# Kernel optimization log

Hardware: AMD Instinct MI355X
Metric: run time of the kernel (lower is better)

Reference implementation:

```python
import jax, jax.numpy as jnp
import numpy as np

_EPS = 1e-5

def _ln(x, g, b):
    m = jnp.mean(x, axis=-1, keepdims=True)
    v = jnp.var(x, axis=-1, keepdims=True)
    return (x - m) * jax.lax.rsqrt(v + _EPS) * g + b

def setup_inputs() -> dict:
    key = jax.random.key(0)
    ks = jax.random.split(key, 12)
    B, S, D = 8, 2048, 1024
    H = 2 * D          # hidden_dim = 2*n_embd
    A = H // 16        # adapt_dim = 128
    E = 8              # num_experts
    std = 1.0 / D ** 0.5
    astd = std * 0.01
    f = lambda k, shape, s: jax.random.normal(k, shape, dtype=jnp.float32) * s
    return {
        'x': f(ks[0], (B, S, D), 1.0),
        'expert_weights': f(ks[1], (B, S, E), 1.0),
        'w_up': f(ks[2], (H, D), std),
        'w_gate': f(ks[3], (H, D), std),
        'w_down': f(ks[4], (D, H), std),
        'w_pre': f(ks[5], (A, D), astd),
        'w_post': f(ks[6], (A, H), astd),
        'an_g': jnp.ones((A,), jnp.float32),
        'an_b': jnp.zeros((A,), jnp.float32),
        'w_aproj': f(ks[7], (H, A), astd),
        'w_exp': f(ks[8], (E, A, A), 0.01 / A ** 0.5),
        'eln_g': jnp.ones((E, A), jnp.float32),
        'eln_b': jnp.zeros((E, A), jnp.float32),
        'w_eproj': f(ks[9], (H, A), 0.01 / A ** 0.5),
        'w_out': f(ks[10], (D, H), 0.01 / A ** 0.5),
    }

def reference(x, expert_weights, w_up, w_gate, w_down, w_pre, w_post,
              an_g, an_b, w_aproj, w_exp, eln_g, eln_b, w_eproj, w_out):
    # ---- shared LLaDAExpert ----
    up = jnp.einsum('bsd,hd->bsh', x, w_up)
    gate = jnp.einsum('bsd,hd->bsh', x, w_gate)
    hidden = jax.nn.silu(gate) * up                      # [B,S,H]
    pre = jnp.einsum('bsd,ad->bsa', x, w_pre)            # pre_adapt(x), reused by experts
    adapt_in = _ln(pre, an_g, an_b)                      # [B,S,A]
    adapt_out = _ln(jnp.einsum('bsh,ah->bsa', hidden, w_post), an_g, an_b)
    aw = jax.nn.silu(jnp.clip(jnp.einsum('bsa,bta->bst', adapt_in, adapt_out), -5.0, 5.0))  # [B,S,S]
    adapt = jnp.einsum('bst,bta->bsa', aw, adapt_in)     # [B,S,A]
    hidden = hidden + 0.1 * jnp.einsum('bsa,ha->bsh', adapt, w_aproj)
    shared = jnp.einsum('bsh,dh->bsd', hidden, w_down)   # [B,S,D]
    combined = jnp.zeros_like(shared)
    E = w_exp.shape[0]
    for i in range(E):
        a = _ln(jnp.einsum('bsa,ca->bsc', pre, w_exp[i]), eln_g[i], eln_b[i])
        o = jnp.einsum('bsh,dh->bsd', jnp.einsum('bsc,hc->bsh', a, w_eproj), w_out)
        mask = expert_weights[:, :, i] > 0
        combined = jnp.where(mask[..., None], o, combined)
    return shared + 0.1 * combined
```

## Files before the change

kernel.cpp:

```cpp
#include <hip/hip_runtime.h>

#define TOK 16384
#define DD 1024
#define HH 2048
#define AA 128
#define EE 8
#define SS 2048
#define BB 8

typedef __attribute__((ext_vector_type(8))) short short8;
typedef __attribute__((ext_vector_type(4))) float floatx4;
typedef __attribute__((address_space(1))) const void glob_cvoid;
typedef __attribute__((address_space(3))) void lds_void;

__device__ __forceinline__ unsigned short f2b(float f) {
  unsigned u = __float_as_uint(f);
  u += 0x7fff + ((u >> 16) & 1);
  return (unsigned short)(u >> 16);
}
__device__ __forceinline__ float b2f(unsigned short h) {
  return __uint_as_float(((unsigned)h) << 16);
}

__device__ __forceinline__ void xcd_swizzle(int& bx, int& by) {
  const int nbx = gridDim.x, nby = gridDim.y;
  if ((nby & 7) == 0) {
    const int L = blockIdx.y * nbx + blockIdx.x;
    const int xcd = L & 7, idx = L >> 3;
    bx = idx % nbx;
    by = (xcd * (nby >> 3)) + idx / nbx;
  } else {
    bx = blockIdx.x; by = blockIdx.y;
  }
}

__global__ void cast_f32_bf16(const float* __restrict__ in, unsigned short* __restrict__ out, long n4) {
  long i = (long)blockIdx.x * blockDim.x + threadIdx.x;
  const long stride = (long)gridDim.x * blockDim.x;
  for (; i < n4; i += stride) {
    float4 v = ((const float4*)in)[i];
    ushort4 o;
    o.x = f2b(v.x); o.y = f2b(v.y); o.z = f2b(v.z); o.w = f2b(v.w);
    ((ushort4*)out)[i] = o;
  }
}

__global__ void transpose_cast(const float* __restrict__ in, unsigned short* __restrict__ out,
                               int R, int C) {
  __shared__ float t[32][33];
  const int lx = threadIdx.x & 31, ly = threadIdx.x >> 5;
  const int r0 = blockIdx.y * 32, c0 = blockIdx.x * 32;
#pragma unroll
  for (int i = 0; i < 32; i += 8)
    t[ly + i][lx] = in[(long)(r0 + ly + i) * C + (c0 + lx)];
  __syncthreads();
#pragma unroll
  for (int i = 0; i < 32; i += 8)
    out[(long)(c0 + ly + i) * R + (r0 + lx)] = f2b(t[lx][ly + i]);
}

template<int EPI>
__global__ __launch_bounds__(256)
void gemm_bt(const unsigned short* __restrict__ Ag, long sAz, int lda,
             const unsigned short* __restrict__ Bg, long sBz, int ldb,
             void* __restrict__ Cg, long sCz, int ldc,
             const unsigned short* __restrict__ Xg, long sXz, int ldx,
             int K)
{
  __shared__ __align__(16) short As[128*64];
  __shared__ __align__(16) short Bs[128*64];
  int bx, by; xcd_swizzle(bx, by);
  const int tid  = threadIdx.x;
  const int lane = tid & 63, wave = tid >> 6;
  const int q = lane >> 4, l15 = lane & 15, l7 = lane & 7;
  const int wm = wave & 1, wn = wave >> 1;

  const int arow = tid >> 3;
  const int kc8  = ((tid & 7) ^ (arow & 7)) * 8;

  const short* Ap = (const short*)Ag + (long)blockIdx.z*sAz + (long)(by*128 + arow)*lda + kc8;
  const short* Bp = (const short*)Bg + (long)blockIdx.z*sBz + (long)(bx*128 + arow)*ldb + kc8;
  char* AsW = (char*)As + wave*1024;
  char* BsW = (char*)Bs + wave*1024;

  floatx4 acc[4][4] = {};

  for (int kt = 0; kt < K; kt += 64) {
    __syncthreads();
#pragma unroll
    for (int i = 0; i < 4; ++i) {
      __builtin_amdgcn_global_load_lds((glob_cvoid*)(Ap + (long)i*32*lda + kt),
                                       (lds_void*)(AsW + i*4096), 16, 0, 0);
      __builtin_amdgcn_global_load_lds((glob_cvoid*)(Bp + (long)i*32*ldb + kt),
                                       (lds_void*)(BsW + i*4096), 16, 0, 0);
    }
    __syncthreads();
#pragma unroll
    for (int s = 0; s < 2; ++s) {
      short8 af[4], bf[4];
      const int slotoff = ((s*4 + q) ^ l7) * 16;
#pragma unroll
      for (int i = 0; i < 4; ++i) {
        af[i] = *(const short8*)((const char*)As + (wm*64 + i*16 + l15)*128 + slotoff);
        bf[i] = *(const short8*)((const char*)Bs + (wn*64 + i*16 + l15)*128 + slotoff);
      }
#pragma unroll
      for (int i = 0; i < 4; ++i)
#pragma unroll
        for (int j = 0; j < 4; ++j)
          acc[i][j] = __builtin_amdgcn_mfma_f32_16x16x32_bf16(af[i], bf[j], acc[i][j], 0, 0, 0);
    }
  }

  const long cz = (long)blockIdx.z * sCz;
  const long xz = (long)blockIdx.z * sXz;
#pragma unroll
  for (int i = 0; i < 4; ++i)
#pragma unroll
    for (int j = 0; j < 4; ++j)
#pragma unroll
      for (int r = 0; r < 4; ++r) {
        const int row = by*128 + wm*64 + i*16 + q*4 + r;
        const int col = bx*128 + wn*64 + j*16 + l15;
        const long ci = cz + (long)row*ldc + col;
        float v = acc[i][j][r];
        if (EPI == 0) {
          ((float*)Cg)[ci] = v;
        } else if (EPI == 1) {
          v = v / (1.f + __expf(-v));
          ((unsigned short*)Cg)[ci] = f2b(v);
        } else if (EPI == 2) {
          float g = b2f(Xg[xz + (long)row*ldx + col]);
          ((unsigned short*)Cg)[ci] = f2b(v * g);
        } else if (EPI == 3) {
          ((unsigned short*)Cg)[ci] = f2b(v);
        } else if (EPI == 4) {
          v = fminf(fmaxf(v, -5.f), 5.f);
          v = v / (1.f + __expf(-v));
          ((unsigned short*)Cg)[ci] = f2b(v);
        } else if (EPI == 6) {
          ((unsigned short*)Cg)[ci] = f2b(0.1f * v);
        }
      }
}

__global__ __launch_bounds__(256)
void gemm_final(const unsigned short* __restrict__ hidp,
                const unsigned short* __restrict__ wdbp,
                const unsigned short* __restrict__ Fcp,
                const unsigned short* __restrict__ Wcp,
                float* __restrict__ outp)
{
  __shared__ __align__(16) short As[128*64];
  __shared__ __align__(16) short Bs[128*64];
  int bx, by; xcd_swizzle(bx, by);
  const int tid  = threadIdx.x;
  const int lane = tid & 63, wave = tid >> 6;
  const int q = lane >> 4, l15 = lane & 15, l7 = lane & 7;
  const int wm = wave & 1, wn = wave >> 1;
  const int arow = tid >> 3;
  const int kc8  = ((tid & 7) ^ (arow & 7)) * 8;
  char* AsW = (char*)As + wave*1024;
  char* BsW = (char*)Bs + wave*1024;

  floatx4 acc[4][4] = {};

  {
    const short* Ap = (const short*)hidp + (long)(by*128 + arow)*HH + kc8;
    const short* Bp = (const short*)wdbp + (long)(bx*128 + arow)*HH + kc8;
    for (int kt = 0; kt < HH; kt += 64) {
      __syncthreads();
#pragma unroll
      for (int i = 0; i < 4; ++i) {
        __builtin_amdgcn_global_load_lds((glob_cvoid*)(Ap + (long)i*32*HH + kt),
                                         (lds_void*)(AsW + i*4096), 16, 0, 0);
        __builtin_amdgcn_global_load_lds((glob_cvoid*)(Bp + (long)i*32*HH + kt),
                                         (lds_void*)(BsW + i*4096), 16, 0, 0);
      }
      __syncthreads();
#pragma unroll
      for (int s = 0; s < 2; ++s) {
        short8 af[4], bf[4];
        const int slotoff = ((s*4 + q) ^ l7) * 16;
#pragma unroll
        for (int i = 0; i < 4; ++i) {
          af[i] = *(const short8*)((const char*)As + (wm*64 + i*16 + l15)*128 + slotoff);
          bf[i] = *(const short8*)((const char*)Bs + (wn*64 + i*16 + l15)*128 + slotoff);
        }
#pragma unroll
        for (int i = 0; i < 4; ++i)
#pragma unroll
          for (int j = 0; j < 4; ++j)
            acc[i][j] = __builtin_amdgcn_mfma_f32_16x16x32_bf16(af[i], bf[j], acc[i][j], 0, 0, 0);
      }
    }
  }
  {
    const short* Ap = (const short*)Fcp + (long)(by*128 + arow)*256 + kc8;
    const short* Bp = (const short*)Wcp + (long)(bx*128 + arow)*256 + kc8;
    for (int kt = 0; kt < 256; kt += 64) {
      __syncthreads();
#pragma unroll
      for (int i = 0; i < 4; ++i) {
        __builtin_amdgcn_global_load_lds((glob_cvoid*)(Ap + (long)i*32*256 + kt),
                                         (lds_void*)(AsW + i*4096), 16, 0, 0);
        __builtin_amdgcn_global_load_lds((glob_cvoid*)(Bp + (long)i*32*256 + kt),
                                         (lds_void*)(BsW + i*4096), 16, 0, 0);
      }
      __syncthreads();
#pragma unroll
      for (int s = 0; s < 2; ++s) {
        short8 af[4], bf[4];
        const int slotoff = ((s*4 + q) ^ l7) * 16;
#pragma unroll
        for (int i = 0; i < 4; ++i) {
          af[i] = *(const short8*)((const char*)As + (wm*64 + i*16 + l15)*128 + slotoff);
          bf[i] = *(const short8*)((const char*)Bs + (wn*64 + i*16 + l15)*128 + slotoff);
        }
#pragma unroll
        for (int i = 0; i < 4; ++i)
#pragma unroll
          for (int j = 0; j < 4; ++j)
            acc[i][j] = __builtin_amdgcn_mfma_f32_16x16x32_bf16(af[i], bf[j], acc[i][j], 0, 0, 0);
      }
    }
  }

#pragma unroll
  for (int i = 0; i < 4; ++i)
#pragma unroll
    for (int j = 0; j < 4; ++j)
#pragma unroll
      for (int r = 0; r < 4; ++r) {
        const int row = by*128 + wm*64 + i*16 + q*4 + r;
        const int col = bx*128 + wn*64 + j*16 + l15;
        outp[(long)row*DD + col] = acc[i][j][r];
      }
}

__global__ void ln_rows(const float* __restrict__ X, const float* __restrict__ g,
                        const float* __restrict__ b, unsigned short* __restrict__ lnout,
                        unsigned short* __restrict__ rawout, unsigned short* __restrict__ tout)
{
  const int lane = threadIdx.x & 63, wave = threadIdx.x >> 6;
  const long t = (long)blockIdx.x*4 + wave;
  const float* x = X + t*AA;
  float x0 = x[lane], x1 = x[lane + 64];
  float s = x0 + x1, s2 = x0*x0 + x1*x1;
#pragma unroll
  for (int m = 1; m < 64; m <<= 1) {
    s  += __shfl_xor(s, m, 64);
    s2 += __shfl_xor(s2, m, 64);
  }
  float mean = s * (1.f/AA);
  float inv  = rsqrtf(s2*(1.f/AA) - mean*mean + 1e-5f);
  float y0 = (x0 - mean)*inv*g[lane] + b[lane];
  float y1 = (x1 - mean)*inv*g[lane+64] + b[lane+64];
  lnout[t*AA + lane]      = f2b(y0);
  lnout[t*AA + lane + 64] = f2b(y1);
  if (rawout) { rawout[t*AA+lane] = f2b(x0); rawout[t*AA+lane+64] = f2b(x1); }
  if (tout) {
    const long bb = t >> 11, si = t & (SS-1);
    tout[bb*(long)AA*SS + (long)lane*SS + si]      = f2b(y0);
    tout[bb*(long)AA*SS + (long)(lane+64)*SS + si] = f2b(y1);
  }
}

__global__ void expert_select_ln(const float* __restrict__ ew, const unsigned short* __restrict__ eall,
                                 const float* __restrict__ eg, const float* __restrict__ ebias,
                                 unsigned short* __restrict__ Fc)
{
  const int lane = threadIdx.x & 63, wave = threadIdx.x >> 6;
  const long t = (long)blockIdx.x*4 + wave;
  const float* w = ew + t*EE;
  int ie = -1;
#pragma unroll
  for (int i = 0; i < EE; ++i) if (w[i] > 0.f) ie = i;
  unsigned short o0 = 0, o1 = 0;
  if (ie >= 0) {
    float x0 = b2f(eall[t*(EE*AA) + ie*AA + lane]);
    float x1 = b2f(eall[t*(EE*AA) + ie*AA + lane + 64]);
    float s = x0 + x1, s2 = x0*x0 + x1*x1;
#pragma unroll
    for (int m = 1; m < 64; m <<= 1) { s += __shfl_xor(s, m, 64); s2 += __shfl_xor(s2, m, 64); }
    float mean = s * (1.f/AA);
    float inv  = rsqrtf(s2*(1.f/AA) - mean*mean + 1e-5f);
    o0 = f2b((x0-mean)*inv*eg[ie*AA+lane]    + ebias[ie*AA+lane]);
    o1 = f2b((x1-mean)*inv*eg[ie*AA+lane+64] + ebias[ie*AA+lane+64]);
  }
  Fc[t*256 + lane]      = o0;
  Fc[t*256 + lane + 64] = o1;
}

extern "C" void kernel_launch(void* const* d_in, const int* in_sizes, int n_in,
                              void* d_out, int out_size, void* d_ws, size_t ws_size,
                              hipStream_t stream)
{
  const float* x       = (const float*)d_in[0];
  const float* ew      = (const float*)d_in[1];
  const float* w_up    = (const float*)d_in[2];
  const float* w_gate  = (const float*)d_in[3];
  const float* w_down  = (const float*)d_in[4];
  const float* w_pre   = (const float*)d_in[5];
  const float* w_post  = (const float*)d_in[6];
  const float* an_g    = (const float*)d_in[7];
  const float* an_b    = (const float*)d_in[8];
  const float* w_aproj = (const float*)d_in[9];
  const float* w_exp   = (const float*)d_in[10];
  const float* eln_g   = (const float*)d_in[11];
  const float* eln_b   = (const float*)d_in[12];
  const float* w_eproj = (const float*)d_in[13];
  const float* w_out   = (const float*)d_in[14];

  char* ws = (char*)d_ws;
  size_t off = 0;
  auto take = [&](size_t bytes) { char* p = ws + off; off += (bytes + 255) & ~(size_t)255; return p; };

  unsigned short* Sc    = (unsigned short*)take((size_t)BB*SS*SS*2);
  unsigned short* xb    = Sc;
  unsigned short* eall  = (unsigned short*)((char*)Sc + (size_t)TOK*DD*2);
  unsigned short* hid   = (unsigned short*)take((size_t)TOK*HH*2);
  float*          pre   = (float*)take((size_t)TOK*AA*4);
  float*          postA = (float*)take((size_t)TOK*AA*4);
  unsigned short* Fc    = (unsigned short*)take((size_t)TOK*256*2);
  unsigned short* ain   = (unsigned short*)take((size_t)TOK*AA*2);
  unsigned short* ainT  = (unsigned short*)take((size_t)TOK*AA*2);
  unsigned short* aout  = (unsigned short*)take((size_t)TOK*AA*2);
  unsigned short* preb  = (unsigned short*)take((size_t)TOK*AA*2);
  unsigned short* wgb   = (unsigned short*)take((size_t)HH*DD*2);
  unsigned short* wub   = (unsigned short*)take((size_t)HH*DD*2);
  unsigned short* wdb   = (unsigned short*)take((size_t)DD*HH*2);
  unsigned short* wpostb= (unsigned short*)take((size_t)AA*HH*2);
  unsigned short* wpreb = (unsigned short*)take((size_t)AA*DD*2);
  unsigned short* wexpb = (unsigned short*)take((size_t)EE*AA*AA*2);
  unsigned short* Wc    = (unsigned short*)take((size_t)DD*256*2);
  (void)ws_size; (void)in_sizes; (void)n_in; (void)out_size;

  unsigned short* woutb  = hid;
  unsigned short* btT    = hid + (size_t)DD*HH;
  unsigned short* eprojT = btT;
  unsigned short* aprojT = btT + (size_t)AA*HH;

  cast_f32_bf16<<<1024, 256, 0, stream>>>(x,      xb,     (long)TOK*DD/4);
  cast_f32_bf16<<<256,  256, 0, stream>>>(w_gate, wgb,    (long)HH*DD/4);
  cast_f32_bf16<<<256,  256, 0, stream>>>(w_up,   wub,    (long)HH*DD/4);
  cast_f32_bf16<<<256,  256, 0, stream>>>(w_down, wdb,    (long)DD*HH/4);
  cast_f32_bf16<<<256,  256, 0, stream>>>(w_out,  woutb,  (long)DD*HH/4);
  cast_f32_bf16<<<64,   256, 0, stream>>>(w_post, wpostb, (long)AA*HH/4);
  cast_f32_bf16<<<32,   256, 0, stream>>>(w_pre,  wpreb,  (long)AA*DD/4);
  cast_f32_bf16<<<32,   256, 0, stream>>>(w_exp,  wexpb,  (long)EE*AA*AA/4);

  transpose_cast<<<dim3(AA/32, HH/32), 256, 0, stream>>>(w_eproj, eprojT, HH, AA);
  transpose_cast<<<dim3(AA/32, HH/32), 256, 0, stream>>>(w_aproj, aprojT, HH, AA);

  gemm_bt<6><<<dim3(1, DD/128, 2), 256, 0, stream>>>(
      woutb, (long)(wdb - woutb), HH,
      eprojT, (long)AA*HH, HH,
      Wc, AA, 256, nullptr, 0, 0, HH);

  gemm_bt<1><<<dim3(HH/128, TOK/128, 1), 256, 0, stream>>>(xb,0,DD, wgb,0,DD, hid,0,HH, nullptr,0,0, DD);
  gemm_bt<2><<<dim3(HH/128, TOK/128, 1), 256, 0, stream>>>(xb,0,DD, wub,0,DD, hid,0,HH, hid,0,HH, DD);

  gemm_bt<0><<<dim3(1, TOK/128, 1), 256, 0, stream>>>(xb,0,DD, wpreb,0,DD, pre,0,AA, nullptr,0,0, DD);
  ln_rows<<<TOK/4, 256, 0, stream>>>(pre, an_g, an_b, ain, preb, ainT);

  gemm_bt<3><<<dim3((EE*AA)/128, TOK/128, 1), 256, 0, stream>>>(preb,0,AA, wexpb,0,AA, eall,0,EE*AA, nullptr,0,0, AA);
  expert_select_ln<<<TOK/4, 256, 0, stream>>>(ew, eall, eln_g, eln_b, Fc);

  gemm_bt<0><<<dim3(1, TOK/128, 1), 256, 0, stream>>>(hid,0,HH, wpostb,0,HH, postA,0,AA, nullptr,0,0, HH);
  ln_rows<<<TOK/4, 256, 0, stream>>>(postA, an_g, an_b, aout, nullptr, nullptr);

  gemm_bt<4><<<dim3(SS/128, SS/128, BB), 256, 0, stream>>>(ain,(long)SS*AA,AA, aout,(long)SS*AA,AA,
                                                           Sc,(long)SS*SS,SS, nullptr,0,0, AA);
  gemm_bt<3><<<dim3(1, SS/128, BB), 256, 0, stream>>>(Sc,(long)SS*SS,SS, ainT,(long)AA*SS,SS,
                                                      Fc+AA,(long)SS*256,256, nullptr,0,0, SS);
  gemm_final<<<dim3(DD/128, TOK/128, 1), 256, 0, stream>>>(hid, wdb, Fc, Wc, (float*)d_out);
}
```

Before: 653.4 us.

## Prefetch next K-tile into registers to overlap global loads with MFMA

```diff
diff --git a/kernel.cpp b/kernel.cpp
--- a/kernel.cpp
+++ b/kernel.cpp
@@ -10,8 +10,6 @@
 
 typedef __attribute__((ext_vector_type(8))) short short8;
 typedef __attribute__((ext_vector_type(4))) float floatx4;
-typedef __attribute__((address_space(1))) const void glob_cvoid;
-typedef __attribute__((address_space(3))) void lds_void;
 
 __device__ __forceinline__ unsigned short f2b(float f) {
   unsigned u = __float_as_uint(f);
@@ -34,6 +32,50 @@
   }
 }
 
+__device__ __forceinline__ void kloop_pipe(const short* Ap, int lda, const short* Bp, int ldb,
+                                           short* As, short* Bs, int K,
+                                           int tid, int q, int l15, int l7, int wm, int wn,
+                                           floatx4 (*acc)[4])
+{
+  short8 pa[4], pb[4];
+#pragma unroll
+  for (int i = 0; i < 4; ++i) {
+    pa[i] = *(const short8*)(Ap + (long)i*32*lda);
+    pb[i] = *(const short8*)(Bp + (long)i*32*ldb);
+  }
+  for (int kt = 0; kt < K; kt += 64) {
+#pragma unroll
+    for (int i = 0; i < 4; ++i) {
+      *(short8*)((char*)As + i*4096 + tid*16) = pa[i];
+      *(short8*)((char*)Bs + i*4096 + tid*16) = pb[i];
+    }
+    __syncthreads();
+    if (kt + 64 < K) {
+#pragma unroll
+      for (int i = 0; i < 4; ++i) {
+        pa[i] = *(const short8*)(Ap + (long)i*32*lda + kt + 64);
+        pb[i] = *(const short8*)(Bp + (long)i*32*ldb + kt + 64);
+      }
+    }
+#pragma unroll
+    for (int s = 0; s < 2; ++s) {
+      short8 af[4], bf[4];
+      const int slotoff = ((s*4 + q) ^ l7) * 16;
+#pragma unroll
+      for (int i = 0; i < 4; ++i) {
+        af[i] = *(const short8*)((const char*)As + (wm*64 + i*16 + l15)*128 + slotoff);
+        bf[i] = *(const short8*)((const char*)Bs + (wn*64 + i*16 + l15)*128 + slotoff);
+      }
+#pragma unroll
+      for (int i = 0; i < 4; ++i)
+#pragma unroll
+        for (int j = 0; j < 4; ++j)
+          acc[i][j] = __builtin_amdgcn_mfma_f32_16x16x32_bf16(af[i], bf[j], acc[i][j], 0, 0, 0);
+    }
+    __syncthreads();
+  }
+}
+
 __global__ void cast_f32_bf16(const float* __restrict__ in, unsigned short* __restrict__ out, long n4) {
   long i = (long)blockIdx.x * blockDim.x + threadIdx.x;
   const long stride = (long)gridDim.x * blockDim.x;
@@ -80,37 +122,9 @@
 
   const short* Ap = (const short*)Ag + (long)blockIdx.z*sAz + (long)(by*128 + arow)*lda + kc8;
   const short* Bp = (const short*)Bg + (long)blockIdx.z*sBz + (long)(bx*128 + arow)*ldb + kc8;
-  char* AsW = (char*)As + wave*1024;
-  char* BsW = (char*)Bs + wave*1024;
 
   floatx4 acc[4][4] = {};
-
-  for (int kt = 0; kt < K; kt += 64) {
-    __syncthreads();
-#pragma unroll
-    for (int i = 0; i < 4; ++i) {
-      __builtin_amdgcn_global_load_lds((glob_cvoid*)(Ap + (long)i*32*lda + kt),
-                                       (lds_void*)(AsW + i*4096), 16, 0, 0);
-      __builtin_amdgcn_global_load_lds((glob_cvoid*)(Bp + (long)i*32*ldb + kt),
-                                       (lds_void*)(BsW + i*4096), 16, 0, 0);
-    }
-    __syncthreads();
-#pragma unroll
-    for (int s = 0; s < 2; ++s) {
-      short8 af[4], bf[4];
-      const int slotoff = ((s*4 + q) ^ l7) * 16;
-#pragma unroll
-      for (int i = 0; i < 4; ++i) {
-        af[i] = *(const short8*)((const char*)As + (wm*64 + i*16 + l15)*128 + slotoff);
-        bf[i] = *(const short8*)((const char*)Bs + (wn*64 + i*16 + l15)*128 + slotoff);
-      }
-#pragma unroll
-      for (int i = 0; i < 4; ++i)
-#pragma unroll
-        for (int j = 0; j < 4; ++j)
-          acc[i][j] = __builtin_amdgcn_mfma_f32_16x16x32_bf16(af[i], bf[j], acc[i][j], 0, 0, 0);
-    }
-  }
+  kloop_pipe(Ap, lda, Bp, ldb, As, Bs, K, tid, q, l15, l7, wm, wn, acc);
 
   const long cz = (long)blockIdx.z * sCz;
   const long xz = (long)blockIdx.z * sXz;
@@ -160,71 +174,15 @@
   const int wm = wave & 1, wn = wave >> 1;
   const int arow = tid >> 3;
   const int kc8  = ((tid & 7) ^ (arow & 7)) * 8;
-  char* AsW = (char*)As + wave*1024;
-  char* BsW = (char*)Bs + wave*1024;
 
   floatx4 acc[4][4] = {};
 
-  {
-    const short* Ap = (const short*)hidp + (long)(by*128 + arow)*HH + kc8;
-    const short* Bp = (const short*)wdbp + (long)(bx*128 + arow)*HH + kc8;
-    for (int kt = 0; kt < HH; kt += 64) {
-      __syncthreads();
-#pragma unroll
-      for (int i = 0; i < 4; ++i) {
-        __builtin_amdgcn_global_load_lds((glob_cvoid*)(Ap + (long)i*32*HH + kt),
-                                         (lds_void*)(AsW + i*4096), 16, 0, 0);
-        __builtin_amdgcn_global_load_lds((glob_cvoid*)(Bp + (long)i*32*HH + kt),
-                                         (lds_void*)(BsW + i*4096), 16, 0, 0);
-      }
-      __syncthreads();
-#pragma unroll
-      for (int s = 0; s < 2; ++s) {
-        short8 af[4], bf[4];
-        const int slotoff = ((s*4 + q) ^ l7) * 16;
-#pragma unroll
-        for (int i = 0; i < 4; ++i) {
-          af[i] = *(const short8*)((const char*)As + (wm*64 + i*16 + l15)*128 + slotoff);
-          bf[i] = *(const short8*)((const char*)Bs + (wn*64 + i*16 + l15)*128 + slotoff);
-        }
-#pragma unroll
-        for (int i = 0; i < 4; ++i)
-#pragma unroll
-          for (int j = 0; j < 4; ++j)
-            acc[i][j] = __builtin_amdgcn_mfma_f32_16x16x32_bf16(af[i], bf[j], acc[i][j], 0, 0, 0);
-      }
-    }
-  }
-  {
-    const short* Ap = (const short*)Fcp + (long)(by*128 + arow)*256 + kc8;
-    const short* Bp = (const short*)Wcp + (long)(bx*128 + arow)*256 + kc8;
-    for (int kt = 0; kt < 256; kt += 64) {
-      __syncthreads();
-#pragma unroll
-      for (int i = 0; i < 4; ++i) {
-        __builtin_amdgcn_global_load_lds((glob_cvoid*)(Ap + (long)i*32*256 + kt),
-                                         (lds_void*)(AsW + i*4096), 16, 0, 0);
-        __builtin_amdgcn_global_load_lds((glob_cvoid*)(Bp + (long)i*32*256 + kt),
-                                         (lds_void*)(BsW + i*4096), 16, 0, 0);
-      }
-      __syncthreads();
-#pragma unroll
-      for (int s = 0; s < 2; ++s) {
-        short8 af[4], bf[4];
-        const int slotoff = ((s*4 + q) ^ l7) * 16;
-#pragma unroll
-        for (int i = 0; i < 4; ++i) {
-          af[i] = *(const short8*)((const char*)As + (wm*64 + i*16 + l15)*128 + slotoff);
-          bf[i] = *(const short8*)((const char*)Bs + (wn*64 + i*16 + l15)*128 + slotoff);
-        }
-#pragma unroll
-        for (int i = 0; i < 4; ++i)
-#pragma unroll
-          for (int j = 0; j < 4; ++j)
-            acc[i][j] = __builtin_amdgcn_mfma_f32_16x16x32_bf16(af[i], bf[j], acc[i][j], 0, 0, 0);
-      }
-    }
-  }
+  kloop_pipe((const short*)hidp + (long)(by*128 + arow)*HH + kc8, HH,
+             (const short*)wdbp + (long)(bx*128 + arow)*HH + kc8, HH,
+             As, Bs, HH, tid, q, l15, l7, wm, wn, acc);
+  kloop_pipe((const short*)Fcp + (long)(by*128 + arow)*256 + kc8, 256,
+             (const short*)Wcp + (long)(bx*128 + arow)*256 + kc8, 256,
+             As, Bs, 256, tid, q, l15, l7, wm, wn, acc);
 
 #pragma unroll
   for (int i = 0; i < 4; ++i)
```

Result: faster. 602.9 us (-7.7%).
